# Optimization experiments

Hardware: AMD Instinct MI355X
Metric: run time of the kernel (lower is better)

## Reference

```python
import jax, jax.numpy as jnp
import numpy as np


def _conv(x, w, b, stride, pad):
    y = jax.lax.conv_general_dilated(x, w, (stride, stride), [(pad, pad), (pad, pad)],
                                     dimension_numbers=('NCHW', 'OIHW', 'NCHW'))
    return y + b[None, :, None, None]


def _deconv(x, w, b, stride):
    # kernel == stride, VALID padding -> exact x`stride` upsample
    y = jax.lax.conv_transpose(x, w, (stride, stride), 'VALID',
                               dimension_numbers=('NCHW', 'OIHW', 'NCHW'))
    return y + b[None, :, None, None]


def _fuse(feat):
    # TransformerFusion: per-pixel scaled dot-product attention over cav axis, keep ego (cav 0)
    n, C, H, W = feat.shape
    t = feat.reshape(n, C, H * W).transpose(2, 0, 1)            # (HW, n, C)
    scores = jnp.einsum('pnc,pmc->pnm', t, t) / np.float32(np.sqrt(C))
    attn = jax.nn.softmax(scores, axis=-1)
    out = jnp.einsum('pnm,pmc->pnc', attn, t)                   # (HW, n, C)
    return out[:, 0, :].T.reshape(C, H, W)


def _sta(x, w1, w2):
    # CBAM-style channel attention: shared MLP on avg-pool and max-pool
    avg = x.mean(axis=(2, 3))                                   # (B, C)
    mx = x.max(axis=(2, 3))
    fc = lambda z: jax.nn.relu(z @ w1.T) @ w2.T
    return jax.nn.sigmoid(fc(avg) + fc(mx))[:, :, None, None]


def _forward(x, historical_x, time_delay, record_len,
             enh_w, enh_b, b0_w, b0_b, b1_w, b1_b, b2_w, b2_b,
             d0_w, d0_b, d1_w, d1_b, d2_w, d2_b, sta_w1, sta_w2):
    aoi = time_delay[0]                                         # (N + 2,)
    enw = jnp.tanh(enh_w * (1.0 / (aoi + 0.1)) + enh_b) + 1.0   # EnhanceWeight, batched
    # loop mapping: t=0 -> x[0]; t=1,2 -> historical[0,1]; t=3,4 -> x[1,2]
    x = x * jnp.stack([enw[0], enw[3], enw[4]])[:, None, None, None]
    historical_x = historical_x * enw[1:3][:, None, None, None]
    historical_x = jax.nn.relu(_conv(historical_x, b0_w, b0_b, 2, 1))  # backbone.blocks[0]

    ups = []
    x = jax.nn.relu(_conv(x, b0_w, b0_b, 2, 1))                 # level 0: (N,64,128,256)
    ups.append(_conv(_fuse(x[:record_len])[None], d0_w, d0_b, 1, 0))
    x = jax.nn.relu(_conv(x, b1_w, b1_b, 2, 1))                 # level 1: (N,128,64,128)
    ups.append(_deconv(_fuse(x[:record_len])[None], d1_w, d1_b, 2))
    x = jax.nn.relu(_conv(x, b2_w, b2_b, 2, 1))                 # level 2: (N,256,32,64)
    ups.append(_deconv(_fuse(x[:record_len])[None], d2_w, d2_b, 4))
    ups.append(historical_x[0:1])
    ups.append(historical_x[1:2])
    x_fuse = jnp.concatenate(ups, axis=1)                       # (1, 512, 128, 256)
    return _sta(x_fuse, sta_w1, sta_w2) * x_fuse


def setup_inputs() -> dict:
    key = jax.random.key(0)
    ks = jax.random.split(key, 16)
    w = lambda k, shape, fan_in: (jax.random.normal(k, shape, jnp.float32)
                                  * np.float32(np.sqrt(2.0 / fan_in)))
    N, C, H, W = 3, 64, 256, 512
    return {
        'x': jax.random.normal(ks[0], (N, C, H, W), jnp.float32),
        'historical_x': jax.random.normal(ks[1], (2, C, H, W), jnp.float32),
        'psm_single': jax.random.normal(ks[2], (N, 2, H // 2, W // 2), jnp.float32),
        'pairwise_t_matrix': jax.random.normal(ks[3], (1, N + 2, N + 2, 4, 4), jnp.float32),
        'time_delay': jax.random.uniform(ks[4], (1, N + 2), jnp.float32),
        'record_len': 3,
        'enh_w': jax.random.normal(ks[5], (), jnp.float32),
        'enh_b': jnp.zeros((), jnp.float32),
        'b0_w': w(ks[6], (64, 64, 3, 3), 64 * 9),  'b0_b': jnp.zeros((64,), jnp.float32),
        'b1_w': w(ks[7], (128, 64, 3, 3), 64 * 9), 'b1_b': jnp.zeros((128,), jnp.float32),
        'b2_w': w(ks[8], (256, 128, 3, 3), 128 * 9), 'b2_b': jnp.zeros((256,), jnp.float32),
        'd0_w': w(ks[9], (128, 64, 1, 1), 64),     'd0_b': jnp.zeros((128,), jnp.float32),
        'd1_w': w(ks[10], (128, 128, 2, 2), 128 * 4), 'd1_b': jnp.zeros((128,), jnp.float32),
        'd2_w': w(ks[11], (128, 256, 4, 4), 256 * 16), 'd2_b': jnp.zeros((128,), jnp.float32),
        'sta_w1': w(ks[12], (32, 512), 512),
        'sta_w2': w(ks[13], (512, 32), 32),
    }


def reference(x, historical_x, psm_single, pairwise_t_matrix, time_delay, record_len,
              enh_w, enh_b, b0_w, b0_b, b1_w, b1_b, b2_w, b2_b,
              d0_w, d0_b, d1_w, d1_b, d2_w, d2_b, sta_w1, sta_w2):
    # psm_single / pairwise_t_matrix are accepted but unused by HPHA's math path
    return _forward(x, historical_x, time_delay, record_len,
                    enh_w, enh_b, b0_w, b0_b, b1_w, b1_b, b2_w, b2_b,
                    d0_w, d0_b, d1_w, d1_b, d2_w, d2_b, sta_w1, sta_w2)
```

## Files before the change

### kernel.cpp

```cpp
#include <hip/hip_runtime.h>
#include <math.h>

#define HW0 32768

typedef __attribute__((ext_vector_type(8))) short short8v;
typedef __attribute__((ext_vector_type(4))) float f32x4;

static const size_t WS_SCALES = 0;
static const size_t WS_MEAN   = 64;
static const size_t WS_MAX    = 64 + 512;
static const size_t WS_GATE   = 64 + 1024;
static const size_t WS_L0X    = 2048;
static const size_t WS_L1     = WS_L0X + (size_t)3*64*128*256;
static const size_t WS_L2     = WS_L1  + (size_t)3*128*64*128;
static const size_t WS_F0     = WS_L2  + (size_t)3*256*32*64;
static const size_t WS_F1     = WS_F0  + (size_t)64*128*256;
static const size_t WS_F2     = WS_F1  + (size_t)128*64*128;
static const size_t WS_W0P    = WS_F2  + (size_t)256*32*64;
static const size_t WS_W1P    = WS_W0P + 18432;
static const size_t WS_W2P    = WS_W1P + 36864;
static const size_t WS_STG    = WS_W2P + 147456;

__device__ inline unsigned short f2bf(float x) {
  unsigned u = __float_as_uint(x);
  unsigned r = ((u >> 16) & 1u) + 0x7FFFu;
  return (unsigned short)((u + r) >> 16);
}

__global__ void prep_k(const float* __restrict__ td, const float* __restrict__ ew,
                       const float* __restrict__ eb, float* __restrict__ scales) {
  int i = threadIdx.x;
  if (i < 5) {
    float e = tanhf(ew[0] * (1.0f / (td[i] + 0.1f)) + eb[0]) + 1.0f;
    const int slot[5] = {0, 3, 4, 1, 2};
    scales[slot[i]] = e;
  }
}

__global__ __launch_bounds__(256) void repack_k(const float* __restrict__ in,
                                                unsigned short* __restrict__ outh,
                                                int C, int H, int W) {
  __shared__ unsigned short lds[64 * 72];
  const int t = threadIdx.x;
  const int cbn = C >> 6;
  const int n  = blockIdx.z / cbn;
  const int cb = (blockIdx.z % cbn) << 6;
  const int h  = blockIdx.y;
  const int w0 = blockIdx.x << 6;
  const int wl = t & 63, cg = t >> 6;
  const float* ip = in + (((size_t)n * C + cb) * H + h) * W + w0;
#pragma unroll 4
  for (int cj = 0; cj < 16; ++cj) {
    int c = cg * 16 + cj;
    lds[wl * 72 + c] = f2bf(ip[(size_t)c * H * W + wl]);
  }
  __syncthreads();
  const int pw = t >> 2, ch = t & 3;
  unsigned short* op = outh + ((size_t)n * H * W + (size_t)h * W + w0 + pw) * C + cb;
#pragma unroll
  for (int it = 0; it < 2; ++it) {
    int c0 = (ch + it * 4) * 8;
    *(uint4*)(op + c0) = *(const uint4*)(lds + pw * 72 + c0);
  }
}

__global__ void pack_w_k(const float* __restrict__ W, unsigned short* __restrict__ wp,
                         int Cout, int Cin, int NK) {
  int t = blockIdx.x * 256 + threadIdx.x;
  if (t >= Cout * NK * 4) return;
  int co = t / (NK * 4); int rem = t - co * (NK * 4); int s = rem >> 2; int js = rem & 3;
  int cog = co >> 4; int l = js * 16 + (co & 15);
  unsigned short v[8];
#pragma unroll
  for (int j = 0; j < 8; ++j) {
    int k = s * 32 + js * 8 + j;
    int tap = k / Cin, ci = k - tap * Cin;
    int ky = tap / 3, kx = tap - ky * 3;
    v[j] = f2bf(W[(((size_t)co * Cin + ci) * 3 + ky) * 3 + kx]);
  }
  *(uint4*)(wp + ((size_t)(cog * NK + s) * 64 + l) * 8) = *(uint4*)v;
}

template <int CIN, int COG>
__global__ __launch_bounds__(256) void conv_mfma_k(
    const unsigned short* __restrict__ inh, const unsigned short* __restrict__ wp,
    const float* __restrict__ bias, float* __restrict__ out,
    const float* __restrict__ scales, int Cout, int Hout, int Wout, int cogrp) {
  constexpr int NK = (9 * CIN) / 32;
  extern __shared__ unsigned short wlds[];
  const int tid = threadIdx.x, lane = tid & 63, wv = tid >> 6;
  const int Hin = Hout * 2, Win = Wout * 2;
  const int n   = blockIdx.z / cogrp;
  const int cg  = blockIdx.z % cogrp;
  const int co0 = cg * (COG * 16);
  const int h   = blockIdx.y;
  const int w0  = blockIdx.x * 64;

  {
    const float4* src = (const float4*)(wp + (size_t)(co0 >> 4) * NK * 64 * 8);
    float4* dst = (float4*)wlds;
    for (int i = tid; i < COG * NK * 64; i += 256) dst[i] = src[i];
  }
  __syncthreads();

  const int px = w0 + wv * 16 + (lane & 15);
  const int js = lane >> 4;
  const unsigned short* inp = inh + (size_t)n * CIN * Hin * Win;

  f32x4 acc[COG];
#pragma unroll
  for (int c = 0; c < COG; ++c) acc[c] = (f32x4){0.f, 0.f, 0.f, 0.f};

  const short8v bz = {0, 0, 0, 0, 0, 0, 0, 0};
  for (int s = 0; s < NK; ++s) {
    const int tap = (s * 32) / CIN;
    const int ci  = (s * 32) % CIN + js * 8;
    const int ky = tap / 3, kx = tap - ky * 3;
    const int iy = 2 * h + ky - 1;
    short8v b = bz;
    if (iy >= 0) {
      const int ix = 2 * px + kx - 1;
      const unsigned short* p = inp + ((size_t)iy * Win + (ix < 0 ? 0 : ix)) * CIN + ci;
      short8v v = *(const short8v*)p;
      if (ix >= 0) b = v;
    }
#pragma unroll
    for (int c = 0; c < COG; ++c) {
      short8v a = *(const short8v*)&wlds[((c * NK + s) * 64 + lane) * 8];
      acc[c] = __builtin_amdgcn_mfma_f32_16x16x32_bf16(a, b, acc[c], 0, 0, 0);
    }
  }

  const float sc = scales ? scales[n] : 1.0f;
#pragma unroll
  for (int c = 0; c < COG; ++c) {
#pragma unroll
    for (int r = 0; r < 4; ++r) {
      const int co = co0 + c * 16 + js * 4 + r;
      float v = fmaxf(acc[c][r] * sc + bias[co], 0.f);
      out[(((size_t)n * Cout + co) * Hout + h) * Wout + px] = v;
    }
  }
}

template <int C>
__global__ __launch_bounds__(256) void fuse2_k(const float* __restrict__ in,
                                               float* __restrict__ out,
                                               int HW, float inv_sqrtC) {
  constexpr int LPP = C / 16;
  constexpr int PPW = 64 / LPP;
  const int tid = threadIdx.x;
  const int lane = tid & 63, wv = tid >> 6;
  const int g = lane / PPW;
  const int p = blockIdx.x * (4 * PPW) + wv * PPW + (lane % PPW);
  const float* b0 = in + (size_t)(g * 16) * HW + p;
  const float* b1 = b0 + (size_t)C * HW;
  const float* b2 = b1 + (size_t)C * HW;
  float va[16], vb[16], vd[16];
  float d00 = 0.f, d01 = 0.f, d02 = 0.f;
#pragma unroll
  for (int j = 0; j < 16; ++j) {
    va[j] = b0[(size_t)j * HW];
    vb[j] = b1[(size_t)j * HW];
    vd[j] = b2[(size_t)j * HW];
    d00 += va[j] * va[j]; d01 += va[j] * vb[j]; d02 += va[j] * vd[j];
  }
#pragma unroll
  for (int off = PPW; off < 64; off <<= 1) {
    d00 += __shfl_xor(d00, off);
    d01 += __shfl_xor(d01, off);
    d02 += __shfl_xor(d02, off);
  }
  float s0 = d00 * inv_sqrtC, s1 = d01 * inv_sqrtC, s2 = d02 * inv_sqrtC;
  float m = fmaxf(s0, fmaxf(s1, s2));
  float e0 = expf(s0 - m), e1 = expf(s1 - m), e2 = expf(s2 - m);
  float inv = 1.0f / (e0 + e1 + e2);
  float a0 = e0 * inv, a1 = e1 * inv, a2 = e2 * inv;
  float* o0 = out + (size_t)(g * 16) * HW + p;
#pragma unroll
  for (int j = 0; j < 16; ++j)
    o0[(size_t)j * HW] = a0 * va[j] + a1 * vb[j] + a2 * vd[j];
}

__global__ __launch_bounds__(256) void up0_k(const float* __restrict__ f,
                                             const float* __restrict__ wgt,
                                             const float* __restrict__ bias,
                                             float* __restrict__ out) {
  const int tid = threadIdx.x, lane = tid & 63, og = tid >> 6;
  const int o0 = blockIdx.y * 16;
  const int p0 = blockIdx.x * 256 + lane;
  __shared__ float wl[64 * 16];
  for (int idx = tid; idx < 1024; idx += 256) {
    int os = idx >> 6, i = idx & 63;
    wl[i * 16 + os] = wgt[(size_t)(o0 + os) * 64 + i];
  }
  __syncthreads();
  float acc[4][4];
#pragma unroll
  for (int k = 0; k < 4; ++k)
#pragma unroll
    for (int j = 0; j < 4; ++j) acc[k][j] = 0.f;
  for (int i = 0; i < 64; ++i) {
    const float* fp = f + (size_t)i * HW0 + p0;
    float4 w4 = *(const float4*)&wl[i * 16 + og * 4];
    float fv[4];
#pragma unroll
    for (int k = 0; k < 4; ++k) fv[k] = fp[k * 64];
#pragma unroll
    for (int k = 0; k < 4; ++k) {
      acc[k][0] += fv[k] * w4.x; acc[k][1] += fv[k] * w4.y;
      acc[k][2] += fv[k] * w4.z; acc[k][3] += fv[k] * w4.w;
    }
  }
#pragma unroll
  for (int j = 0; j < 4; ++j) {
    const int o = o0 + og * 4 + j;
    const float b = bias[o];
    float* op = out + (size_t)o * HW0 + p0;
#pragma unroll
    for (int k = 0; k < 4; ++k) op[k * 64] = acc[k][j] + b;
  }
}

__global__ __launch_bounds__(256) void up1_k(const float* __restrict__ f,
                                             const float* __restrict__ wgt,
                                             const float* __restrict__ bias,
                                             float* __restrict__ out) {
  const int tid = threadIdx.x, lane = tid & 63, og = tid >> 6;
  const int o0 = blockIdx.y * 8;
  const int h = blockIdx.x;
  const int c = lane & 1;
  const int wbase = lane >> 1;
  __shared__ float wl[128 * 4 * 8];
  for (int idx = tid; idx < 128 * 4 * 8; idx += 256) {
    int os = idx >> 9;
    int rem = idx & 511;
    int i = rem >> 2, rc = rem & 3;
    wl[(i * 4 + rc) * 8 + os] = wgt[((size_t)(o0 + os) * 128 + i) * 4 + rc];
  }
  __syncthreads();
  float acc[2][2][4];
#pragma unroll
  for (int j = 0; j < 2; ++j)
#pragma unroll
    for (int r = 0; r < 2; ++r)
#pragma unroll
      for (int k = 0; k < 4; ++k) acc[j][r][k] = 0.f;
  const int rc_r0 = 2 + (1 - c);
  const int rc_r1 = (1 - c);
  for (int i = 0; i < 128; ++i) {
    const float* frow = f + ((size_t)i * 64 + h) * 128;
    float fv[4];
#pragma unroll
    for (int k = 0; k < 4; ++k) fv[k] = frow[wbase + 32 * k];
    float2 w0 = *(const float2*)&wl[(i * 4 + rc_r0) * 8 + og * 2];
    float2 w1 = *(const float2*)&wl[(i * 4 + rc_r1) * 8 + og * 2];
#pragma unroll
    for (int k = 0; k < 4; ++k) {
      acc[0][0][k] += fv[k] * w0.x; acc[1][0][k] += fv[k] * w0.y;
      acc[0][1][k] += fv[k] * w1.x; acc[1][1][k] += fv[k] * w1.y;
    }
  }
#pragma unroll
  for (int j = 0; j < 2; ++j) {
    const int o = o0 + og * 2 + j;
    const float b = bias[o];
#pragma unroll
    for (int r = 0; r < 2; ++r) {
      float* op = out + (size_t)o * HW0 + (size_t)(2 * h + r) * 256 + lane;
#pragma unroll
      for (int k = 0; k < 4; ++k) op[64 * k] = acc[j][r][k] + b;
    }
  }
}

__global__ __launch_bounds__(256) void up2_k(const float* __restrict__ f,
                                             const float* __restrict__ wgt,
                                             const float* __restrict__ bias,
                                             float* __restrict__ out) {
  const int tid = threadIdx.x, lane = tid & 63, og = tid >> 6;
  const int o0 = blockIdx.y * 4;
  const int h = blockIdx.x;
  const int c = lane & 3;
  const int wbase = lane >> 2;
  __shared__ float wl[256 * 16 * 4];
  for (int idx = tid; idx < 256 * 16 * 4; idx += 256) {
    int os = idx >> 12;
    int rem = idx & 4095;
    int i = rem >> 4, rc = rem & 15;
    wl[(i * 16 + rc) * 4 + os] = wgt[((size_t)(o0 + os) * 256 + i) * 16 + rc];
  }
  __syncthreads();
  float acc[4][4];
#pragma unroll
  for (int r = 0; r < 4; ++r)
#pragma unroll
    for (int k = 0; k < 4; ++k) acc[r][k] = 0.f;
  for (int i = 0; i < 256; ++i) {
    const float* frow = f + ((size_t)i * 32 + h) * 64;
    float fv[4];
#pragma unroll
    for (int k = 0; k < 4; ++k) fv[k] = frow[wbase + 16 * k];
    float wv[4];
#pragma unroll
    for (int r = 0; r < 4; ++r) wv[r] = wl[(i * 16 + (3 - r) * 4 + (3 - c)) * 4 + og];
#pragma unroll
    for (int r = 0; r < 4; ++r)
#pragma unroll
      for (int k = 0; k < 4; ++k) acc[r][k] += fv[k] * wv[r];
  }
  const int o = o0 + og;
  const float b = bias[o];
#pragma unroll
  for (int r = 0; r < 4; ++r) {
    float* op = out + (size_t)o * HW0 + (size_t)(4 * h + r) * 256 + lane;
#pragma unroll
    for (int k = 0; k < 4; ++k) op[64 * k] = acc[r][k] + b;
  }
}

__global__ __launch_bounds__(256) void sta_reduce_k(const float* __restrict__ xf,
                                                    float* __restrict__ mean,
                                                    float* __restrict__ mx) {
  const int c = blockIdx.x;
  const float* p = xf + (size_t)c * HW0;
  float s = 0.f, m = -1e30f;
  for (int i = threadIdx.x * 4; i < HW0; i += 1024) {
    float4 v = *(const float4*)(p + i);
    s += v.x + v.y + v.z + v.w;
    m = fmaxf(m, fmaxf(fmaxf(v.x, v.y), fmaxf(v.z, v.w)));
  }
#pragma unroll
  for (int off = 32; off; off >>= 1) {
    s += __shfl_down(s, off);
    m = fmaxf(m, __shfl_down(m, off));
  }
  __shared__ float ss[4], sm[4];
  if ((threadIdx.x & 63) == 0) { ss[threadIdx.x >> 6] = s; sm[threadIdx.x >> 6] = m; }
  __syncthreads();
  if (threadIdx.x == 0) {
    float S = ss[0] + ss[1] + ss[2] + ss[3];
    float M = fmaxf(fmaxf(sm[0], sm[1]), fmaxf(sm[2], sm[3]));
    mean[c] = S * (1.0f / 32768.0f);
    mx[c] = M;
  }
}

__global__ void sta_gate_k(const float* __restrict__ mean, const float* __restrict__ mx,
                           const float* __restrict__ w1, const float* __restrict__ w2,
                           float* __restrict__ gate) {
  __shared__ float havg[32], hmax[32];
  const int t = threadIdx.x;
  if (t < 32) {
    float sa = 0.f, sm = 0.f;
    for (int cc = 0; cc < 512; ++cc) {
      float w = w1[t * 512 + cc];
      sa += mean[cc] * w;
      sm += mx[cc] * w;
    }
    havg[t] = fmaxf(sa, 0.f);
    hmax[t] = fmaxf(sm, 0.f);
  }
  __syncthreads();
  float g = 0.f;
  for (int j = 0; j < 32; ++j) g += (havg[j] + hmax[j]) * w2[t * 32 + j];
  gate[t] = 1.0f / (1.0f + expf(-g));
}

__global__ __launch_bounds__(256) void sta_scale_k(float* __restrict__ xf,
                                                   const float* __restrict__ gate) {
  const size_t i = (size_t)(blockIdx.x * 256 + threadIdx.x) * 4;
  float4 v = *(const float4*)(xf + i);
  const float g = gate[i >> 15];
  v.x *= g; v.y *= g; v.z *= g; v.w *= g;
  *(float4*)(xf + i) = v;
}

extern "C" void kernel_launch(void* const* d_in, const int* in_sizes, int n_in,
                              void* d_out, int out_size, void* d_ws, size_t ws_size,
                              hipStream_t stream) {
  const float* x    = (const float*)d_in[0];
  const float* hist = (const float*)d_in[1];
  const float* td   = (const float*)d_in[4];
  const float* ew   = (const float*)d_in[6];
  const float* eb   = (const float*)d_in[7];
  const float* b0w  = (const float*)d_in[8];
  const float* b0b  = (const float*)d_in[9];
  const float* b1w  = (const float*)d_in[10];
  const float* b1b  = (const float*)d_in[11];
  const float* b2w  = (const float*)d_in[12];
  const float* b2b  = (const float*)d_in[13];
  const float* d0w  = (const float*)d_in[14];
  const float* d0b  = (const float*)d_in[15];
  const float* d1w  = (const float*)d_in[16];
  const float* d1b  = (const float*)d_in[17];
  const float* d2w  = (const float*)d_in[18];
  const float* d2b  = (const float*)d_in[19];
  const float* w1   = (const float*)d_in[20];
  const float* w2   = (const float*)d_in[21];

  float* out = (float*)d_out;
  float* ws  = (float*)d_ws;

  float* scales = ws + WS_SCALES;
  float* l0x = ws + WS_L0X;
  float* l1  = ws + WS_L1;
  float* l2  = ws + WS_L2;
  float* f0  = ws + WS_F0;
  float* f1  = ws + WS_F1;
  float* f2  = ws + WS_F2;
  unsigned short* w0p = (unsigned short*)(ws + WS_W0P);
  unsigned short* w1p = (unsigned short*)(ws + WS_W1P);
  unsigned short* w2p = (unsigned short*)(ws + WS_W2P);
  unsigned short* stg = (unsigned short*)(ws + WS_STG);

  prep_k<<<1, 64, 0, stream>>>(td, ew, eb, scales);
  pack_w_k<<<18, 256, 0, stream>>>(b0w, w0p, 64, 64, 18);
  pack_w_k<<<36, 256, 0, stream>>>(b1w, w1p, 128, 64, 18);
  pack_w_k<<<144, 256, 0, stream>>>(b2w, w2p, 256, 128, 36);

  repack_k<<<dim3(8, 256, 3), 256, 0, stream>>>(x, stg, 64, 256, 512);
  conv_mfma_k<64, 4><<<dim3(4, 128, 3), 256, 73728, stream>>>(
      stg, w0p, b0b, l0x, scales, 64, 128, 256, 1);

  repack_k<<<dim3(8, 256, 2), 256, 0, stream>>>(hist, stg, 64, 256, 512);
  conv_mfma_k<64, 4><<<dim3(4, 128, 2), 256, 73728, stream>>>(
      stg, w0p, b0b, out + (size_t)384 * HW0, scales + 3, 64, 128, 256, 1);

  fuse2_k<64><<<512, 256, 0, stream>>>(l0x, f0, 32768, 0.125f);
  up0_k<<<dim3(128, 8), 256, 0, stream>>>(f0, d0w, d0b, out);

  repack_k<<<dim3(4, 128, 3), 256, 0, stream>>>(l0x, stg, 64, 128, 256);
  conv_mfma_k<64, 4><<<dim3(2, 64, 6), 256, 73728, stream>>>(
      stg, w1p, b1b, l1, nullptr, 128, 64, 128, 2);
  fuse2_k<128><<<256, 256, 0, stream>>>(l1, f1, 8192, 0.0883883476f);
  up1_k<<<dim3(64, 16), 256, 0, stream>>>(f1, d1w, d1b, out + (size_t)128 * HW0);

  repack_k<<<dim3(2, 64, 6), 256, 0, stream>>>(l1, stg, 128, 64, 128);
  conv_mfma_k<128, 2><<<dim3(1, 32, 24), 256, 73728, stream>>>(
      stg, w2p, b2b, l2, nullptr, 256, 32, 64, 8);
  fuse2_k<256><<<128, 256, 0, stream>>>(l2, f2, 2048, 0.0625f);
  up2_k<<<dim3(32, 32), 256, 0, stream>>>(f2, d2w, d2b, out + (size_t)256 * HW0);

  sta_reduce_k<<<512, 256, 0, stream>>>(out, ws + WS_MEAN, ws + WS_MAX);
  sta_gate_k<<<1, 512, 0, stream>>>(ws + WS_MEAN, ws + WS_MAX, w1, w2, ws + WS_GATE);
  sta_scale_k<<<16384, 256, 0, stream>>>(out, ws + WS_GATE);
}
```

Measured before the change: 585.9 us.

## Run upsample convs and deconvs as bf16 MFMA GEMMs on pixel-major fused features

```diff
diff --git a/kernel.cpp b/kernel.cpp
--- a/kernel.cpp
+++ b/kernel.cpp
@@ -19,7 +19,10 @@
 static const size_t WS_W0P    = WS_F2  + (size_t)256*32*64;
 static const size_t WS_W1P    = WS_W0P + 18432;
 static const size_t WS_W2P    = WS_W1P + 36864;
-static const size_t WS_STG    = WS_W2P + 147456;
+static const size_t WS_U0P    = WS_W2P + 147456;
+static const size_t WS_U1P    = WS_U0P + 4096;
+static const size_t WS_U2P    = WS_U1P + 32768;
+static const size_t WS_STG    = WS_U2P + 262144;
 
 __device__ inline unsigned short f2bf(float x) {
   unsigned u = __float_as_uint(x);
@@ -81,6 +84,31 @@
   *(uint4*)(wp + ((size_t)(cog * NK + s) * 64 + l) * 8) = *(uint4*)v;
 }
 
+__global__ void pack_dw_k(const float* __restrict__ W, unsigned short* __restrict__ wp,
+                          int M, int K, int NK, int mode) {
+  int t = blockIdx.x * 256 + threadIdx.x;
+  if (t >= M * NK * 4) return;
+  int m = t / (NK * 4); int rem = t - m * (NK * 4); int s = rem >> 2; int js = rem & 3;
+  int mt = m >> 4; int l = js * 16 + (m & 15);
+  unsigned short v[8];
+#pragma unroll
+  for (int j = 0; j < 8; ++j) {
+    int k = s * 32 + js * 8 + j;
+    size_t idx;
+    if (mode == 0) {
+      idx = (size_t)m * K + k;
+    } else if (mode == 1) {
+      int o = m >> 2, r = (m >> 1) & 1, c = m & 1;
+      idx = ((size_t)o * K + k) * 4 + (1 - r) * 2 + (1 - c);
+    } else {
+      int o = m >> 4, r = (m >> 2) & 3, c = m & 3;
+      idx = ((size_t)o * K + k) * 16 + (3 - r) * 4 + (3 - c);
+    }
+    v[j] = f2bf(W[idx]);
+  }
+  *(uint4*)(wp + ((size_t)(mt * NK + s) * 64 + l) * 8) = *(uint4*)v;
+}
+
 template <int CIN, int COG>
 __global__ __launch_bounds__(256) void conv_mfma_k(
     const unsigned short* __restrict__ inh, const unsigned short* __restrict__ wp,
@@ -145,7 +173,7 @@
 
 template <int C>
 __global__ __launch_bounds__(256) void fuse2_k(const float* __restrict__ in,
-                                               float* __restrict__ out,
+                                               unsigned short* __restrict__ outh,
                                                int HW, float inv_sqrtC) {
   constexpr int LPP = C / 16;
   constexpr int PPW = 64 / LPP;
@@ -176,146 +204,75 @@
   float e0 = expf(s0 - m), e1 = expf(s1 - m), e2 = expf(s2 - m);
   float inv = 1.0f / (e0 + e1 + e2);
   float a0 = e0 * inv, a1 = e1 * inv, a2 = e2 * inv;
-  float* o0 = out + (size_t)(g * 16) * HW + p;
+  unsigned short tmp[16];
 #pragma unroll
   for (int j = 0; j < 16; ++j)
-    o0[(size_t)j * HW] = a0 * va[j] + a1 * vb[j] + a2 * vd[j];
-}
-
-__global__ __launch_bounds__(256) void up0_k(const float* __restrict__ f,
-                                             const float* __restrict__ wgt,
-                                             const float* __restrict__ bias,
-                                             float* __restrict__ out) {
-  const int tid = threadIdx.x, lane = tid & 63, og = tid >> 6;
-  const int o0 = blockIdx.y * 16;
-  const int p0 = blockIdx.x * 256 + lane;
-  __shared__ float wl[64 * 16];
-  for (int idx = tid; idx < 1024; idx += 256) {
-    int os = idx >> 6, i = idx & 63;
-    wl[i * 16 + os] = wgt[(size_t)(o0 + os) * 64 + i];
+    tmp[j] = f2bf(a0 * va[j] + a1 * vb[j] + a2 * vd[j]);
+  unsigned short* o0 = outh + (size_t)p * C + g * 16;
+  *(uint4*)(o0)     = *(const uint4*)(tmp);
+  *(uint4*)(o0 + 8) = *(const uint4*)(tmp + 8);
+}
+
+template <int K, int MT, int EPI>
+__global__ __launch_bounds__(256) void up_mfma_k(
+    const unsigned short* __restrict__ fh, const unsigned short* __restrict__ wp,
+    const float* __restrict__ bias, float* __restrict__ out) {
+  constexpr int NK = K / 32;
+  extern __shared__ unsigned short wlds[];
+  const int tid = threadIdx.x, lane = tid & 63, wv = tid >> 6;
+  const int mt0 = blockIdx.y * MT;
+  {
+    const float4* src = (const float4*)(wp + (size_t)mt0 * NK * 64 * 8);
+    float4* dst = (float4*)wlds;
+    for (int i = tid; i < MT * NK * 64; i += 256) dst[i] = src[i];
   }
   __syncthreads();
-  float acc[4][4];
-#pragma unroll
-  for (int k = 0; k < 4; ++k)
-#pragma unroll
-    for (int j = 0; j < 4; ++j) acc[k][j] = 0.f;
-  for (int i = 0; i < 64; ++i) {
-    const float* fp = f + (size_t)i * HW0 + p0;
-    float4 w4 = *(const float4*)&wl[i * 16 + og * 4];
-    float fv[4];
-#pragma unroll
-    for (int k = 0; k < 4; ++k) fv[k] = fp[k * 64];
-#pragma unroll
-    for (int k = 0; k < 4; ++k) {
-      acc[k][0] += fv[k] * w4.x; acc[k][1] += fv[k] * w4.y;
-      acc[k][2] += fv[k] * w4.z; acc[k][3] += fv[k] * w4.w;
-    }
-  }
-#pragma unroll
-  for (int j = 0; j < 4; ++j) {
-    const int o = o0 + og * 4 + j;
-    const float b = bias[o];
-    float* op = out + (size_t)o * HW0 + p0;
-#pragma unroll
-    for (int k = 0; k < 4; ++k) op[k * 64] = acc[k][j] + b;
-  }
-}
-
-__global__ __launch_bounds__(256) void up1_k(const float* __restrict__ f,
-                                             const float* __restrict__ wgt,
-                                             const float* __restrict__ bias,
-                                             float* __restrict__ out) {
-  const int tid = threadIdx.x, lane = tid & 63, og = tid >> 6;
-  const int o0 = blockIdx.y * 8;
-  const int h = blockIdx.x;
-  const int c = lane & 1;
-  const int wbase = lane >> 1;
-  __shared__ float wl[128 * 4 * 8];
-  for (int idx = tid; idx < 128 * 4 * 8; idx += 256) {
-    int os = idx >> 9;
-    int rem = idx & 511;
-    int i = rem >> 2, rc = rem & 3;
-    wl[(i * 4 + rc) * 8 + os] = wgt[((size_t)(o0 + os) * 128 + i) * 4 + rc];
-  }
-  __syncthreads();
-  float acc[2][2][4];
-#pragma unroll
-  for (int j = 0; j < 2; ++j)
-#pragma unroll
-    for (int r = 0; r < 2; ++r)
-#pragma unroll
-      for (int k = 0; k < 4; ++k) acc[j][r][k] = 0.f;
-  const int rc_r0 = 2 + (1 - c);
-  const int rc_r1 = (1 - c);
-  for (int i = 0; i < 128; ++i) {
-    const float* frow = f + ((size_t)i * 64 + h) * 128;
-    float fv[4];
-#pragma unroll
-    for (int k = 0; k < 4; ++k) fv[k] = frow[wbase + 32 * k];
-    float2 w0 = *(const float2*)&wl[(i * 4 + rc_r0) * 8 + og * 2];
-    float2 w1 = *(const float2*)&wl[(i * 4 + rc_r1) * 8 + og * 2];
-#pragma unroll
-    for (int k = 0; k < 4; ++k) {
-      acc[0][0][k] += fv[k] * w0.x; acc[1][0][k] += fv[k] * w0.y;
-      acc[0][1][k] += fv[k] * w1.x; acc[1][1][k] += fv[k] * w1.y;
-    }
-  }
-#pragma unroll
-  for (int j = 0; j < 2; ++j) {
-    const int o = o0 + og * 2 + j;
-    const float b = bias[o];
-#pragma unroll
-    for (int r = 0; r < 2; ++r) {
-      float* op = out + (size_t)o * HW0 + (size_t)(2 * h + r) * 256 + lane;
-#pragma unroll
-      for (int k = 0; k < 4; ++k) op[64 * k] = acc[j][r][k] + b;
-    }
-  }
-}
-
-__global__ __launch_bounds__(256) void up2_k(const float* __restrict__ f,
-                                             const float* __restrict__ wgt,
-                                             const float* __restrict__ bias,
-                                             float* __restrict__ out) {
-  const int tid = threadIdx.x, lane = tid & 63, og = tid >> 6;
-  const int o0 = blockIdx.y * 4;
-  const int h = blockIdx.x;
-  const int c = lane & 3;
-  const int wbase = lane >> 2;
-  __shared__ float wl[256 * 16 * 4];
-  for (int idx = tid; idx < 256 * 16 * 4; idx += 256) {
-    int os = idx >> 12;
-    int rem = idx & 4095;
-    int i = rem >> 4, rc = rem & 15;
-    wl[(i * 16 + rc) * 4 + os] = wgt[((size_t)(o0 + os) * 256 + i) * 16 + rc];
-  }
-  __syncthreads();
-  float acc[4][4];
-#pragma unroll
-  for (int r = 0; r < 4; ++r)
-#pragma unroll
-    for (int k = 0; k < 4; ++k) acc[r][k] = 0.f;
-  for (int i = 0; i < 256; ++i) {
-    const float* frow = f + ((size_t)i * 32 + h) * 64;
-    float fv[4];
-#pragma unroll
-    for (int k = 0; k < 4; ++k) fv[k] = frow[wbase + 16 * k];
-    float wv[4];
-#pragma unroll
-    for (int r = 0; r < 4; ++r) wv[r] = wl[(i * 16 + (3 - r) * 4 + (3 - c)) * 4 + og];
-#pragma unroll
-    for (int r = 0; r < 4; ++r)
-#pragma unroll
-      for (int k = 0; k < 4; ++k) acc[r][k] += fv[k] * wv[r];
-  }
-  const int o = o0 + og;
-  const float b = bias[o];
-#pragma unroll
-  for (int r = 0; r < 4; ++r) {
-    float* op = out + (size_t)o * HW0 + (size_t)(4 * h + r) * 256 + lane;
-#pragma unroll
-    for (int k = 0; k < 4; ++k) op[64 * k] = acc[r][k] + b;
+
+  const int px = blockIdx.x * 64 + wv * 16 + (lane & 15);
+  const int js = lane >> 4;
+  const unsigned short* bp = fh + (size_t)px * K + js * 8;
+
+  f32x4 acc[MT];
+#pragma unroll
+  for (int t = 0; t < MT; ++t) acc[t] = (f32x4){0.f, 0.f, 0.f, 0.f};
+
+#pragma unroll
+  for (int s = 0; s < NK; ++s) {
+    short8v b = *(const short8v*)(bp + s * 32);
+#pragma unroll
+    for (int t = 0; t < MT; ++t) {
+      short8v a = *(const short8v*)&wlds[((t * NK + s) * 64 + lane) * 8];
+      acc[t] = __builtin_amdgcn_mfma_f32_16x16x32_bf16(a, b, acc[t], 0, 0, 0);
+    }
+  }
+
+  if constexpr (EPI == 0) {
+#pragma unroll
+    for (int t = 0; t < MT; ++t) {
+      const int o = (mt0 + t) * 16 + js * 4;
+#pragma unroll
+      for (int r = 0; r < 4; ++r)
+        out[(size_t)(o + r) * HW0 + px] = acc[t][r] + bias[o + r];
+    }
+  } else if constexpr (EPI == 1) {
+    const int h = px >> 7, w = px & 127;
+#pragma unroll
+    for (int t = 0; t < MT; ++t) {
+      const int o = (mt0 + t) * 4 + js;
+      const float b = bias[o];
+      float* base = out + (size_t)o * HW0 + (size_t)(2 * h) * 256 + 2 * w;
+      *(float2*)base         = make_float2(acc[t][0] + b, acc[t][1] + b);
+      *(float2*)(base + 256) = make_float2(acc[t][2] + b, acc[t][3] + b);
+    }
+  } else {
+    const int h = px >> 6, w = px & 63;
+#pragma unroll
+    for (int t = 0; t < MT; ++t) {
+      const int o = mt0 + t;
+      const float b = bias[o];
+      float4 v = make_float4(acc[t][0] + b, acc[t][1] + b, acc[t][2] + b, acc[t][3] + b);
+      *(float4*)(out + (size_t)o * HW0 + (size_t)(4 * h + js) * 256 + 4 * w) = v;
+    }
   }
 }
 
@@ -406,18 +363,24 @@
   float* l0x = ws + WS_L0X;
   float* l1  = ws + WS_L1;
   float* l2  = ws + WS_L2;
-  float* f0  = ws + WS_F0;
-  float* f1  = ws + WS_F1;
-  float* f2  = ws + WS_F2;
+  unsigned short* f0h = (unsigned short*)(ws + WS_F0);
+  unsigned short* f1h = (unsigned short*)(ws + WS_F1);
+  unsigned short* f2h = (unsigned short*)(ws + WS_F2);
   unsigned short* w0p = (unsigned short*)(ws + WS_W0P);
   unsigned short* w1p = (unsigned short*)(ws + WS_W1P);
   unsigned short* w2p = (unsigned short*)(ws + WS_W2P);
+  unsigned short* u0p = (unsigned short*)(ws + WS_U0P);
+  unsigned short* u1p = (unsigned short*)(ws + WS_U1P);
+  unsigned short* u2p = (unsigned short*)(ws + WS_U2P);
   unsigned short* stg = (unsigned short*)(ws + WS_STG);
 
   prep_k<<<1, 64, 0, stream>>>(td, ew, eb, scales);
   pack_w_k<<<18, 256, 0, stream>>>(b0w, w0p, 64, 64, 18);
   pack_w_k<<<36, 256, 0, stream>>>(b1w, w1p, 128, 64, 18);
   pack_w_k<<<144, 256, 0, stream>>>(b2w, w2p, 256, 128, 36);
+  pack_dw_k<<<4, 256, 0, stream>>>(d0w, u0p, 128, 64, 2, 0);
+  pack_dw_k<<<32, 256, 0, stream>>>(d1w, u1p, 512, 128, 4, 1);
+  pack_dw_k<<<256, 256, 0, stream>>>(d2w, u2p, 2048, 256, 8, 2);
 
   repack_k<<<dim3(8, 256, 3), 256, 0, stream>>>(x, stg, 64, 256, 512);
   conv_mfma_k<64, 4><<<dim3(4, 128, 3), 256, 73728, stream>>>(
@@ -427,20 +390,22 @@
   conv_mfma_k<64, 4><<<dim3(4, 128, 2), 256, 73728, stream>>>(
       stg, w0p, b0b, out + (size_t)384 * HW0, scales + 3, 64, 128, 256, 1);
 
-  fuse2_k<64><<<512, 256, 0, stream>>>(l0x, f0, 32768, 0.125f);
-  up0_k<<<dim3(128, 8), 256, 0, stream>>>(f0, d0w, d0b, out);
+  fuse2_k<64><<<512, 256, 0, stream>>>(l0x, f0h, 32768, 0.125f);
+  up_mfma_k<64, 8, 0><<<dim3(512, 1), 256, 16384, stream>>>(f0h, u0p, d0b, out);
 
   repack_k<<<dim3(4, 128, 3), 256, 0, stream>>>(l0x, stg, 64, 128, 256);
   conv_mfma_k<64, 4><<<dim3(2, 64, 6), 256, 73728, stream>>>(
       stg, w1p, b1b, l1, nullptr, 128, 64, 128, 2);
-  fuse2_k<128><<<256, 256, 0, stream>>>(l1, f1, 8192, 0.0883883476f);
-  up1_k<<<dim3(64, 16), 256, 0, stream>>>(f1, d1w, d1b, out + (size_t)128 * HW0);
+  fuse2_k<128><<<256, 256, 0, stream>>>(l1, f1h, 8192, 0.0883883476f);
+  up_mfma_k<128, 8, 1><<<dim3(128, 4), 256, 32768, stream>>>(
+      f1h, u1p, d1b, out + (size_t)128 * HW0);
 
   repack_k<<<dim3(2, 64, 6), 256, 0, stream>>>(l1, stg, 128, 64, 128);
   conv_mfma_k<128, 2><<<dim3(1, 32, 24), 256, 73728, stream>>>(
       stg, w2p, b2b, l2, nullptr, 256, 32, 64, 8);
-  fuse2_k<256><<<128, 256, 0, stream>>>(l2, f2, 2048, 0.0625f);
-  up2_k<<<dim3(32, 32), 256, 0, stream>>>(f2, d2w, d2b, out + (size_t)256 * HW0);
+  fuse2_k<256><<<128, 256, 0, stream>>>(l2, f2h, 2048, 0.0625f);
+  up_mfma_k<256, 4, 2><<<dim3(32, 32), 256, 32768, stream>>>(
+      f2h, u2p, d2b, out + (size_t)256 * HW0);
 
   sta_reduce_k<<<512, 256, 0, stream>>>(out, ws + WS_MEAN, ws + WS_MAX);
   sta_gate_k<<<1, 512, 0, stream>>>(ws + WS_MEAN, ws + WS_MAX, w1, w2, ws + WS_GATE);
```

Result: faster. 505.1 us (-13.8%).
